# Kernel tuning notes

Hardware: AMD Instinct MI355X
Metric: run time of the kernel (lower is better)

## Reference

```python
import jax, jax.numpy as jnp
import numpy as np
from jax import lax

B, L, D, E, K, H = 8, 1024, 256, 8, 2, 1024  # batch, seq(in_channel), in_dim, experts, top_k, out_channel/hidden
LMAX = L // 2  # largest expert input dim (factor i+2 = 2)
LENS = [L // (i + 2) for i in range(E)]


def setup_inputs() -> dict:
    key = jax.random.key(0)
    ks = jax.random.split(key, 12)
    x = jax.random.normal(ks[0], (B, L, D), dtype=jnp.float32)
    conv_ws = jax.random.normal(ks[1], (3, D, D, 3), dtype=jnp.float32) / np.sqrt(3 * D)
    conv_bs = jax.random.normal(ks[2], (3, D), dtype=jnp.float32) * 0.01
    fl_w = jax.random.normal(ks[3], (E, L), dtype=jnp.float32) / np.sqrt(L)
    fl_b = jax.random.normal(ks[4], (E,), dtype=jnp.float32) * 0.01
    # expert first-layer weights, zero-padded on input axis to LMAX (expert i uses L//(i+2) inputs)
    w1 = jax.random.normal(ks[5], (E, H, LMAX), dtype=jnp.float32) / np.sqrt(LMAX)
    col_mask = (np.arange(LMAX)[None, :] < np.array(LENS)[:, None]).astype(np.float32)  # [E, LMAX]
    w1 = w1 * jnp.asarray(col_mask)[:, None, :]
    b1 = jax.random.normal(ks[6], (E, H), dtype=jnp.float32) * 0.01
    w2 = jax.random.normal(ks[7], (E, H, H), dtype=jnp.float32) / np.sqrt(H)
    b2 = jax.random.normal(ks[8], (E, H), dtype=jnp.float32) * 0.01
    w3 = jax.random.normal(ks[9], (E, H, H), dtype=jnp.float32) / np.sqrt(H)
    b3 = jax.random.normal(ks[10], (E, H), dtype=jnp.float32) * 0.01
    return {"x": x, "conv_ws": conv_ws, "conv_bs": conv_bs, "fl_w": fl_w, "fl_b": fl_b,
            "w1": w1, "b1": b1, "w2": w2, "b2": b2, "w3": w3, "b3": b3}


def _gelu(v):
    return jax.nn.gelu(v, approximate=False)  # torch nn.GELU default is exact erf


def _forward(x, conv_ws, conv_bs, fl_w, fl_b, w1, b1, w2, b2, w3, b3):
    xt = jnp.transpose(x, (0, 2, 1))  # [B, D, L]
    # --- Router: 3 dilated causal-padded ('same') convs + GELU ---
    h = xt
    for i in range(3):
        d = 2 ** i
        h = lax.conv_general_dilated(h, conv_ws[i], window_strides=(1,), padding=[(d, d)],
                                     rhs_dilation=(d,), dimension_numbers=("NCH", "OIH", "NCH"))
        h = _gelu(h + conv_bs[i][None, :, None])
    logits = jax.nn.sigmoid(jnp.einsum("bdl,el->bde", h, fl_w) + fl_b)  # [B, D, E]
    prob = jax.nn.softmax(logits, axis=-1)
    top_val, top_idx = lax.top_k(prob, K)  # [B, D, K]
    top_val = top_val / jnp.sum(top_val, axis=-1, keepdims=True)
    # combine gate per expert: gates[b,d,e] = sum_k top_val * 1[top_idx==e]
    gates = jnp.sum(top_val[..., None] * jax.nn.one_hot(top_idx, E, dtype=top_val.dtype), axis=2)  # [B, D, E]
    # --- Per-expert downsample (avg_pool1d, kernel=stride=i+2), zero-padded to LMAX ---
    xs = []
    for i in range(E):
        f = i + 2
        Li = LENS[i]
        xd = xt[:, :, :Li * f].reshape(B, D, Li, f).mean(-1)  # [B, D, Li]
        xs.append(jnp.pad(xd, ((0, 0), (0, 0), (0, LMAX - Li))))
    xe = jnp.stack(xs)  # [E, B, D, LMAX]; pad cols align with zeroed w1 cols
    # --- Expert MLPs (dense compute, masked by gates; zero gate == token not routed) ---
    h1 = _gelu(jnp.einsum("ebdl,ehl->ebdh", xe, w1) + b1[:, None, None, :])
    h2 = _gelu(jnp.einsum("ebdh,egh->ebdg", h1, w2) + b2[:, None, None, :])
    h3 = jnp.einsum("ebdg,eog->ebdo", h2, w3) + b3[:, None, None, :]  # [E, B, D, H]
    out = jnp.einsum("ebdo,bde->bdo", h3, gates)  # scatter-add combine, [B, D, H]
    return jnp.transpose(out, (0, 2, 1))  # [B, L(out_channel), D]


def reference(x, conv_ws, conv_bs, fl_w, fl_b, w1, b1, w2, b2, w3, b3):
    return _forward(x, conv_ws, conv_bs, fl_w, fl_b, w1, b1, w2, b2, w3, b3)
```

## Files before the change

kernel.cpp:

```cpp
#include <hip/hip_runtime.h>
#include <math.h>

#define Bb 8
#define Ll 1024
#define Dd 256
#define Ee 8
#define Hh 1024
#define LMAXc 512
#define NTOK (Bb*Dd)
#define LPAD 1032
#define MAXTILES 72

typedef short bf16x8 __attribute__((ext_vector_type(8)));
typedef float f32x4 __attribute__((ext_vector_type(4)));
typedef unsigned short u16x8 __attribute__((ext_vector_type(8)));

__device__ __forceinline__ float gelu_f(float x) {
    return 0.5f * x * (1.0f + erff(x * 0.70710678118654752440f));
}
__device__ __forceinline__ unsigned short f2b(float x) {
    unsigned int u = __float_as_uint(x);
    return (unsigned short)((u + 0x7fffu + ((u >> 16) & 1u)) >> 16);
}
__device__ __forceinline__ float b2f(unsigned short h) {
    return __uint_as_float(((unsigned int)h) << 16);
}
__device__ __forceinline__ void gl_lds16(const void* g, void* l) {
    __builtin_amdgcn_global_load_lds((const __attribute__((address_space(1))) unsigned int*)g,
                                     (__attribute__((address_space(3))) unsigned int*)l, 16, 0, 0);
}
__device__ __forceinline__ void split_one4(const float* __restrict__ src,
                                           unsigned short* __restrict__ hi,
                                           unsigned short* __restrict__ lo, int idx) {
    float4 v = ((const float4*)src)[idx];
    ushort2 h01, h23, l01, l23;
    unsigned short h;
    h = f2b(v.x); h01.x = h; l01.x = f2b(v.x - b2f(h));
    h = f2b(v.y); h01.y = h; l01.y = f2b(v.y - b2f(h));
    h = f2b(v.z); h23.x = h; l23.x = f2b(v.z - b2f(h));
    h = f2b(v.w); h23.y = h; l23.y = f2b(v.w - b2f(h));
    ((ushort2*)hi)[idx * 2] = h01; ((ushort2*)hi)[idx * 2 + 1] = h23;
    ((ushort2*)lo)[idx * 2] = l01; ((ushort2*)lo)[idx * 2 + 1] = l23;
}
__device__ __forceinline__ void cvt_one4(const float* __restrict__ src,
                                         unsigned short* __restrict__ dst, int idx) {
    float4 v = ((const float4*)src)[idx];
    ushort2 h01, h23;
    h01.x = f2b(v.x); h01.y = f2b(v.y);
    h23.x = f2b(v.z); h23.y = f2b(v.w);
    ((ushort2*)dst)[idx * 2] = h01; ((ushort2*)dst)[idx * 2 + 1] = h23;
}

__global__ __launch_bounds__(256) void prep_all(
    const float* __restrict__ x, const float* __restrict__ cw,
    const float* __restrict__ w1, const float* __restrict__ w2,
    const float* __restrict__ w3,
    unsigned short* __restrict__ xhi, unsigned short* __restrict__ xlo,
    unsigned short* __restrict__ chi, unsigned short* __restrict__ clo,
    unsigned short* __restrict__ wchi, unsigned short* __restrict__ wclo,
    unsigned short* __restrict__ w1hi, unsigned short* __restrict__ w1lo,
    unsigned short* __restrict__ w2b, unsigned short* __restrict__ w3b)
{
    int blk = blockIdx.x;
    int t = threadIdx.x;
    if (blk < 2048) {
        int idx = blk * 256 + t;
        int d4 = idx & 63;
        int l  = (idx >> 6) & 1023;
        int b  = idx >> 16;
        float4 v = ((const float4*)x)[idx];
        size_t o = ((size_t)(b * LPAD + 4 + l) * Dd + d4 * 4) >> 1;
        ushort2 h01, h23, l01, l23;
        unsigned short h;
        h = f2b(v.x); h01.x = h; l01.x = f2b(v.x - b2f(h));
        h = f2b(v.y); h01.y = h; l01.y = f2b(v.y - b2f(h));
        h = f2b(v.z); h23.x = h; l23.x = f2b(v.z - b2f(h));
        h = f2b(v.w); h23.y = h; l23.y = f2b(v.w - b2f(h));
        ((ushort2*)xhi)[o] = h01; ((ushort2*)xhi)[o + 1] = h23;
        ((ushort2*)xlo)[o] = l01; ((ushort2*)xlo)[o + 1] = l23;
    } else if (blk < 4352) {
        int idx = (blk - 2048) * 256 + t;
        int i = idx & (Dd - 1);
        int o = (idx >> 8) & (Dd - 1);
        int lk = idx >> 16;
        int layer = lk / 3;
        int k = lk % 3;
        float v = cw[(((size_t)layer * Dd + o) * Dd + i) * 3 + k];
        unsigned short h = f2b(v);
        wchi[idx] = h;
        wclo[idx] = f2b(v - b2f(h));
    } else if (blk < 8448) {
        split_one4(w1, w1hi, w1lo, (blk - 4352) * 256 + t);
    } else if (blk < 16640) {
        cvt_one4(w2, w2b, (blk - 8448) * 256 + t);
    } else if (blk < 24832) {
        cvt_one4(w3, w3b, (blk - 16640) * 256 + t);
    } else {
        int u = (blk - 24832) * 256 + t;
        int f = u >> 11;
        int rem = u & 2047;
        int b = rem >> 8;
        int r2 = rem & 255;
        int row = r2 >> 5;
        int col = (r2 & 31) * 8;
        int padrow = (row < 4) ? row : (1024 + row);
        unsigned short* buf = (f == 0) ? xhi : (f == 1) ? xlo : (f == 2) ? chi : clo;
        u16x8 z = {0, 0, 0, 0, 0, 0, 0, 0};
        *(u16x8*)(buf + (size_t)(b * LPAD + padrow) * Dd + col) = z;
    }
}

template<int MODE>
__global__ __launch_bounds__(256, 2) void conv_mfma(
    const unsigned short* __restrict__ inhi, const unsigned short* __restrict__ inlo,
    const unsigned short* __restrict__ whiL, const unsigned short* __restrict__ wloL,
    const float* __restrict__ bias,
    unsigned short* __restrict__ outhi, unsigned short* __restrict__ outlo,
    float* __restrict__ outf, int dil)
{
    __shared__ char smem[32768];
    char* sAhi = smem;
    char* sAlo = smem + 8192;
    char* sBhi = smem + 16384;
    char* sBlo = smem + 24576;

    const int t = threadIdx.x;
    const int lane = t & 63, w = t >> 6;
    const int r16 = lane & 15, quad = lane >> 4;
    const int wr = w >> 1, wc = w & 1;
    const int row0 = blockIdx.x * 64;
    const int col0 = blockIdx.y * 64;
    const int b = row0 >> 10, l0 = row0 & 1023;

    int aoff[2], boff[2];
    #pragma unroll
    for (int i = 0; i < 2; ++i) {
        int ra = wr * 32 + i * 16 + r16;
        aoff[i] = ra * 64 + ((quad ^ ((ra >> 1) & 3)) << 4);
        int rb = wc * 32 + i * 16 + r16;
        boff[i] = rb * 64 + ((quad ^ ((rb >> 1) & 3)) << 4);
    }
    const int rs = t >> 2, ce = ((t & 3) ^ ((rs >> 1) & 3)) << 3;
    const unsigned short* gAhi = inhi + (size_t)(b * LPAD + 4 + l0 + rs) * Dd + ce;
    const unsigned short* gAlo = inlo + (size_t)(b * LPAD + 4 + l0 + rs) * Dd + ce;

    f32x4 acc[2][2];
    const f32x4 zero4 = {0.f, 0.f, 0.f, 0.f};
    #pragma unroll
    for (int i = 0; i < 2; ++i)
        #pragma unroll
        for (int j = 0; j < 2; ++j) acc[i][j] = zero4;

    for (int tap = 0; tap < 3; ++tap) {
        const int sh = (tap - 1) * dil;
        const unsigned short* pAhi = gAhi + sh * Dd;
        const unsigned short* pAlo = gAlo + sh * Dd;
        const unsigned short* gBhi = whiL + ((size_t)tap * Dd + col0 + rs) * Dd + ce;
        const unsigned short* gBlo = wloL + ((size_t)tap * Dd + col0 + rs) * Dd + ce;
        for (int kb = 0; kb < Dd; kb += 64) {
            gl_lds16(pAhi + kb,      sAhi + (w << 10));
            gl_lds16(pAhi + kb + 32, sAhi + 4096 + (w << 10));
            gl_lds16(pAlo + kb,      sAlo + (w << 10));
            gl_lds16(pAlo + kb + 32, sAlo + 4096 + (w << 10));
            gl_lds16(gBhi + kb,      sBhi + (w << 10));
            gl_lds16(gBhi + kb + 32, sBhi + 4096 + (w << 10));
            gl_lds16(gBlo + kb,      sBlo + (w << 10));
            gl_lds16(gBlo + kb + 32, sBlo + 4096 + (w << 10));
            __syncthreads();
            #pragma unroll
            for (int h = 0; h < 2; ++h) {
                const int ho = h * 4096;
                bf16x8 ah[2], al[2], bh[2], bl[2];
                #pragma unroll
                for (int i = 0; i < 2; ++i) {
                    ah[i] = *(const bf16x8*)(sAhi + ho + aoff[i]);
                    al[i] = *(const bf16x8*)(sAlo + ho + aoff[i]);
                    bh[i] = *(const bf16x8*)(sBhi + ho + boff[i]);
                    bl[i] = *(const bf16x8*)(sBlo + ho + boff[i]);
                }
                #pragma unroll
                for (int mi = 0; mi < 2; ++mi)
                    #pragma unroll
                    for (int ni = 0; ni < 2; ++ni) {
                        acc[mi][ni] = __builtin_amdgcn_mfma_f32_16x16x32_bf16(ah[mi], bh[ni], acc[mi][ni], 0, 0, 0);
                        acc[mi][ni] = __builtin_amdgcn_mfma_f32_16x16x32_bf16(ah[mi], bl[ni], acc[mi][ni], 0, 0, 0);
                        acc[mi][ni] = __builtin_amdgcn_mfma_f32_16x16x32_bf16(al[mi], bh[ni], acc[mi][ni], 0, 0, 0);
                    }
            }
            __syncthreads();
        }
    }

    int cc[2]; float bv[2];
    #pragma unroll
    for (int ni = 0; ni < 2; ++ni) {
        cc[ni] = col0 + wc * 32 + ni * 16 + r16;
        bv[ni] = bias[cc[ni]];
    }
    #pragma unroll
    for (int mi = 0; mi < 2; ++mi) {
        int lb = l0 + wr * 32 + mi * 16 + quad * 4;
        #pragma unroll
        for (int reg = 0; reg < 4; ++reg) {
            int l = lb + reg;
            #pragma unroll
            for (int ni = 0; ni < 2; ++ni) {
                float v = gelu_f(acc[mi][ni][reg] + bv[ni]);
                if (MODE == 0) {
                    size_t o = (size_t)(b * LPAD + 4 + l) * Dd + cc[ni];
                    unsigned short h = f2b(v);
                    outhi[o] = h;
                    outlo[o] = f2b(v - b2f(h));
                } else {
                    outf[(size_t)(b * Ll + l) * Dd + cc[ni]] = v;
                }
            }
        }
    }
}

template<int MODE, int GATHER, int TWOPASS>
__global__ __launch_bounds__(256, 4) void gemm_sp(
    const unsigned short* __restrict__ AG,
    const unsigned short* __restrict__ BhiG, const unsigned short* __restrict__ BloG,
    const float* __restrict__ biasG, const float* __restrict__ gates,
    const int* __restrict__ cntG, const int* __restrict__ listG,
    const int* __restrict__ tileTab, const int* __restrict__ ntiles,
    unsigned short* __restrict__ Cout, float* __restrict__ outf,
    int M, int N, int K)
{
    if (blockIdx.y >= ntiles[0]) return;
    const int desc = tileTab[blockIdx.y];
    const int e = desc >> 16;
    const int row0 = (desc & 0xffff) * 64;
    const int cn = cntG[e];

    __shared__ char smem[TWOPASS ? 40960 : 24576];
    char* sA   = smem;
    char* sBhi = smem + 8192;
    char* sBlo = smem + 24576;

    const unsigned short* Bhi = BhiG + (size_t)e * N * K;
    const unsigned short* Blo = TWOPASS ? (BloG + (size_t)e * N * K) : nullptr;
    const float* bias = biasG + (size_t)e * N;

    const int t = threadIdx.x;
    const int lane = t & 63, w = t >> 6;
    const int r16 = lane & 15, quad = lane >> 4;
    const int wr = w >> 1, wc = w & 1;
    const int col0 = blockIdx.x * 128;

    int aoff[2], boff[4];
    #pragma unroll
    for (int i = 0; i < 2; ++i) {
        int ra = wr * 32 + i * 16 + r16;
        aoff[i] = ra * 64 + ((quad ^ ((ra >> 1) & 3)) << 4);
    }
    #pragma unroll
    for (int j = 0; j < 4; ++j) {
        int rb = wc * 64 + j * 16 + r16;
        boff[j] = rb * 64 + ((quad ^ ((rb >> 1) & 3)) << 4);
    }
    const int r0s = t >> 2, c0s = ((t & 3) ^ ((r0s >> 1) & 3)) << 3;
    const int r1s = r0s + 64, c1s = ((t & 3) ^ ((r1s >> 1) & 3)) << 3;
    int ri = row0 + r0s; if (ri > cn - 1) ri = cn - 1;
    const int ar = GATHER ? listG[e * NTOK + ri] : ri;
    const unsigned short* gA  = AG + ((size_t)e * M + ar) * K + c0s;
    const unsigned short* gBhi0 = Bhi + (size_t)(col0 + r0s) * K + c0s;
    const unsigned short* gBhi1 = Bhi + (size_t)(col0 + r1s) * K + c1s;
    const unsigned short* gBlo0 = TWOPASS ? (Blo + (size_t)(col0 + r0s) * K + c0s) : nullptr;
    const unsigned short* gBlo1 = TWOPASS ? (Blo + (size_t)(col0 + r1s) * K + c1s) : nullptr;
    const int wofs = w << 10;

    f32x4 acc[2][4];
    const f32x4 zero4 = {0.f, 0.f, 0.f, 0.f};
    #pragma unroll
    for (int i = 0; i < 2; ++i)
        #pragma unroll
        for (int j = 0; j < 4; ++j) acc[i][j] = zero4;

    for (int k0 = 0; k0 < K; k0 += 64) {
        gl_lds16(gA + k0,          sA + wofs);
        gl_lds16(gA + k0 + 32,     sA + 4096 + wofs);
        gl_lds16(gBhi0 + k0,       sBhi + wofs);
        gl_lds16(gBhi1 + k0,       sBhi + 4096 + wofs);
        gl_lds16(gBhi0 + k0 + 32,  sBhi + 8192 + wofs);
        gl_lds16(gBhi1 + k0 + 32,  sBhi + 12288 + wofs);
        if (TWOPASS) {
            gl_lds16(gBlo0 + k0,       sBlo + wofs);
            gl_lds16(gBlo1 + k0,       sBlo + 4096 + wofs);
            gl_lds16(gBlo0 + k0 + 32,  sBlo + 8192 + wofs);
            gl_lds16(gBlo1 + k0 + 32,  sBlo + 12288 + wofs);
        }
        __syncthreads();
        #pragma unroll
        for (int h = 0; h < 2; ++h) {
            const int ao = h * 4096, bo = h * 8192;
            bf16x8 ah[2], bh[4];
            #pragma unroll
            for (int i = 0; i < 2; ++i) ah[i] = *(const bf16x8*)(sA + ao + aoff[i]);
            #pragma unroll
            for (int j = 0; j < 4; ++j) bh[j] = *(const bf16x8*)(sBhi + bo + boff[j]);
            #pragma unroll
            for (int mi = 0; mi < 2; ++mi)
                #pragma unroll
                for (int ni = 0; ni < 4; ++ni)
                    acc[mi][ni] = __builtin_amdgcn_mfma_f32_16x16x32_bf16(ah[mi], bh[ni], acc[mi][ni], 0, 0, 0);
            if (TWOPASS) {
                bf16x8 bl[4];
                #pragma unroll
                for (int j = 0; j < 4; ++j) bl[j] = *(const bf16x8*)(sBlo + bo + boff[j]);
                #pragma unroll
                for (int mi = 0; mi < 2; ++mi)
                    #pragma unroll
                    for (int ni = 0; ni < 4; ++ni)
                        acc[mi][ni] = __builtin_amdgcn_mfma_f32_16x16x32_bf16(ah[mi], bl[ni], acc[mi][ni], 0, 0, 0);
            }
        }
        __syncthreads();
    }

    int cc[4]; float bv[4];
    #pragma unroll
    for (int ni = 0; ni < 4; ++ni) {
        cc[ni] = col0 + wc * 64 + ni * 16 + r16;
        bv[ni] = bias[cc[ni]];
    }
    if (MODE == 0) {
        unsigned short* CE = Cout + (size_t)e * M * N;
        #pragma unroll
        for (int mi = 0; mi < 2; ++mi) {
            int rb = row0 + wr * 32 + mi * 16 + quad * 4;
            #pragma unroll
            for (int reg = 0; reg < 4; ++reg) {
                size_t roff = (size_t)(rb + reg) * N;
                #pragma unroll
                for (int ni = 0; ni < 4; ++ni)
                    CE[roff + cc[ni]] = f2b(gelu_f(acc[mi][ni][reg] + bv[ni]));
            }
        }
    } else {
        #pragma unroll
        for (int mi = 0; mi < 2; ++mi) {
            int rb = row0 + wr * 32 + mi * 16 + quad * 4;
            #pragma unroll
            for (int reg = 0; reg < 4; ++reg) {
                int i = rb + reg;
                if (i < cn) {
                    int tok = listG[e * NTOK + i];
                    float g = gates[(size_t)tok * Ee + e];
                    size_t roff = (size_t)tok * N;
                    #pragma unroll
                    for (int ni = 0; ni < 4; ++ni)
                        atomicAdd(&outf[roff + cc[ni]], g * (acc[mi][ni][reg] + bv[ni]));
                }
            }
        }
    }
}


__global__ __launch_bounds__(256) void logits_accum(const float* __restrict__ h,
                                                    const float* __restrict__ fl_w,
                                                    float* __restrict__ logits) {
    int b = blockIdx.x;
    int chunk = blockIdx.y;
    __shared__ float wsm[Ee][128];
    for (int i = threadIdx.x; i < Ee * 128; i += 256) {
        int e = i >> 7, l = i & 127;
        wsm[e][l] = fl_w[e * Ll + chunk * 128 + l];
    }
    __syncthreads();
    int d = threadIdx.x;
    float acc[Ee] = {};
    for (int l = 0; l < 128; ++l) {
        float v = h[((size_t)b * Ll + chunk * 128 + l) * Dd + d];
        #pragma unroll
        for (int e = 0; e < Ee; ++e) acc[e] += v * wsm[e][l];
    }
    int tok = b * Dd + d;
    #pragma unroll
    for (int e = 0; e < Ee; ++e) atomicAdd(&logits[tok * Ee + e], acc[e]);
}

__global__ __launch_bounds__(1024) void gates_final(const float* __restrict__ logits,
                                                    const float* __restrict__ fl_b,
                                                    float* __restrict__ gates,
                                                    int* __restrict__ cnt,
                                                    int* __restrict__ list,
                                                    int* __restrict__ tileTab,
                                                    int* __restrict__ ntiles) {
    for (int tok = threadIdx.x; tok < NTOK; tok += 1024) {
        float s[Ee];
        #pragma unroll
        for (int e = 0; e < Ee; ++e) {
            float z = logits[tok * Ee + e] + fl_b[e];
            s[e] = 1.0f / (1.0f + expf(-z));
        }
        float mx = s[0];
        #pragma unroll
        for (int e = 1; e < Ee; ++e) mx = fmaxf(mx, s[e]);
        float p[Ee];
        #pragma unroll
        for (int e = 0; e < Ee; ++e) p[e] = expf(s[e] - mx);
        int i1 = 0;
        #pragma unroll
        for (int e = 1; e < Ee; ++e) if (p[e] > p[i1]) i1 = e;
        int i2 = (i1 == 0) ? 1 : 0;
        #pragma unroll
        for (int e = 0; e < Ee; ++e) {
            if (e == i1 || e == i2) continue;
            if (p[e] > p[i2]) i2 = e;
        }
        float inv = 1.0f / (p[i1] + p[i2]);
        #pragma unroll
        for (int e = 0; e < Ee; ++e) gates[tok * Ee + e] = 0.0f;
        gates[tok * Ee + i1] = p[i1] * inv;
        gates[tok * Ee + i2] = p[i2] * inv;
        int p1 = atomicAdd(&cnt[i1], 1);
        list[i1 * NTOK + p1] = tok;
        int p2 = atomicAdd(&cnt[i2], 1);
        list[i2 * NTOK + p2] = tok;
    }
    __syncthreads();
    if (threadIdx.x == 0) {
        int nt = 0;
        for (int e = 0; e < Ee; ++e) {
            int c = atomicAdd(&cnt[e], 0);
            for (int m = 0; m * 64 < c; ++m) tileTab[nt++] = (e << 16) | m;
        }
        ntiles[0] = nt;
    }
}

__global__ __launch_bounds__(256) void downsample_v3(const float* __restrict__ x,
                                                     unsigned short* __restrict__ xe) {
    int e = blockIdx.z;
    int f = e + 2;
    int Li = Ll / f;
    int j0 = blockIdx.x * 8;
    if (j0 >= Li) return;
    int b = blockIdx.y;
    int d = threadIdx.x;
    float invf = 1.0f / (float)f;
    int lim = Li - 1;
    float v[8] = {};
    for (int r = 0; r < f; ++r) {
        #pragma unroll
        for (int jj = 0; jj < 8; ++jj) {
            int j = j0 + jj; if (j > lim) j = lim;
            v[jj] += x[((size_t)(b * Ll + j * f + r)) * Dd + d];
        }
    }
    size_t obase = ((size_t)(e * NTOK + b * 256 + d)) * LMAXc + j0;
    if (j0 + 8 <= Li) {
        u16x8 hv;
        #pragma unroll
        for (int q = 0; q < 8; ++q) hv[q] = (short)f2b(v[q] * invf);
        *(u16x8*)(xe + obase) = hv;
    } else {
        for (int jj = 0; jj < Li - j0; ++jj)
            xe[obase + jj] = f2b(v[jj] * invf);
    }
}

__global__ __launch_bounds__(256) void transpose_out(const float* __restrict__ outacc,
                                                     float* __restrict__ out) {
    __shared__ float tile[32][33];
    int b = blockIdx.z;
    int d0 = blockIdx.x * 32;
    int o0 = blockIdx.y * 32;
    int tx = threadIdx.x & 31, ty = threadIdx.x >> 5;
    for (int i = 0; i < 32; i += 8)
        tile[ty + i][tx] = outacc[((size_t)b * Dd + d0 + ty + i) * Hh + o0 + tx];
    __syncthreads();
    for (int i = 0; i < 32; i += 8)
        out[((size_t)b * Hh + o0 + ty + i) * Dd + d0 + tx] = tile[tx][ty + i];
}

extern "C" void kernel_launch(void* const* d_in, const int* in_sizes, int n_in,
                              void* d_out, int out_size, void* d_ws, size_t ws_size,
                              hipStream_t stream) {
    const float* x       = (const float*)d_in[0];
    const float* conv_w  = (const float*)d_in[1];
    const float* conv_b  = (const float*)d_in[2];
    const float* fl_w    = (const float*)d_in[3];
    const float* fl_b    = (const float*)d_in[4];
    const float* w1      = (const float*)d_in[5];
    const float* b1      = (const float*)d_in[6];
    const float* w2      = (const float*)d_in[7];
    const float* b2      = (const float*)d_in[8];
    const float* w3      = (const float*)d_in[9];
    const float* b3      = (const float*)d_in[10];
    float* out = (float*)d_out;

    char* ws = (char*)d_ws;
    unsigned short* xphi = (unsigned short*)(ws);
    unsigned short* xplo = (unsigned short*)(ws + 4227072);
    unsigned short* cphi = (unsigned short*)(ws + 8454144);
    unsigned short* cplo = (unsigned short*)(ws + 12681216);
    unsigned short* wchi = (unsigned short*)(ws + 16908288);
    unsigned short* wclo = (unsigned short*)(ws + 18087936);
    float* hL            = (float*)(ws + 19267584);
    unsigned short* h1   = (unsigned short*)(ws);
    unsigned short* h2   = (unsigned short*)(ws + 33554432);
    unsigned short* xe   = (unsigned short*)(ws + 67108864);
    unsigned short* w1hi = (unsigned short*)(ws + 83886080);
    unsigned short* w1lo = (unsigned short*)(ws + 92274688);
    unsigned short* w2b  = (unsigned short*)(ws + 100663296);
    unsigned short* w3b  = (unsigned short*)(ws + 117440512);
    float* logits  = (float*)(ws + 134217728);
    int*   cnt     = (int*)(ws + 134283264);
    int*   ntiles  = (int*)(ws + 134283296);
    int*   tileTab = (int*)(ws + 134283328);
    float* gates   = (float*)(ws + 134284288);
    int*   list    = (int*)(ws + 134349824);
    float* outacc  = (float*)(ws);

    hipMemsetAsync(logits, 0, 65536 + 64, stream);

    prep_all<<<24864, 256, 0, stream>>>(x, conv_w, w1, w2, w3,
                                        xphi, xplo, cphi, cplo, wchi, wclo,
                                        w1hi, w1lo, w2b, w3b);

    const int WL = 3 * Dd * Dd;
    conv_mfma<0><<<dim3(Bb * Ll / 64, Dd / 64), 256, 0, stream>>>(
        xphi, xplo, wchi + 0 * WL, wclo + 0 * WL, conv_b + 0 * Dd, cphi, cplo, nullptr, 1);
    conv_mfma<0><<<dim3(Bb * Ll / 64, Dd / 64), 256, 0, stream>>>(
        cphi, cplo, wchi + 1 * WL, wclo + 1 * WL, conv_b + 1 * Dd, xphi, xplo, nullptr, 2);
    conv_mfma<1><<<dim3(Bb * Ll / 64, Dd / 64), 256, 0, stream>>>(
        xphi, xplo, wchi + 2 * WL, wclo + 2 * WL, conv_b + 2 * Dd, nullptr, nullptr, hL, 4);

    logits_accum<<<dim3(Bb, 8), 256, 0, stream>>>(hL, fl_w, logits);
    gates_final<<<1, 1024, 0, stream>>>(logits, fl_b, gates, cnt, list, tileTab, ntiles);

    downsample_v3<<<dim3(64, Bb, Ee), 256, 0, stream>>>(x, xe);

    gemm_sp<0, 1, 1><<<dim3(Hh / 128, MAXTILES), 256, 0, stream>>>(
        xe, w1hi, w1lo, b1, nullptr, cnt, list, tileTab, ntiles, h1, nullptr, NTOK, Hh, LMAXc);

    gemm_sp<0, 0, 0><<<dim3(Hh / 128, MAXTILES), 256, 0, stream>>>(
        h1, w2b, nullptr, b2, nullptr, cnt, list, tileTab, ntiles, h2, nullptr, NTOK, Hh, Hh);

    hipMemsetAsync(outacc, 0, (size_t)NTOK * Hh * sizeof(float), stream);

    gemm_sp<1, 0, 0><<<dim3(Hh / 128, MAXTILES), 256, 0, stream>>>(
        h2, w3b, nullptr, b3, gates, cnt, list, tileTab, ntiles, nullptr, outacc, NTOK, Hh, Hh);

    transpose_out<<<dim3(Dd / 32, Hh / 32, Bb), 256, 0, stream>>>(outacc, out);
}
```

Baseline: 329.1 us.

## Halve expert GEMM column tile and aggregate routing atomics per wavefront

The expert GEMM kernels now use 64x64 output tiles instead of 64x128, doubling the grid width to 16 column blocks so more workgroups are available for the sparse tile count. Shared memory per block shrinks accordingly. The routing kernel replaces per-token global atomics with wavefront ballot aggregation into shared-memory counters, writing the counts out once at the end. The smaller tile gives less B-operand reuse per A load and doubles A-tile reloads.

```diff
diff --git a/kernel.cpp b/kernel.cpp
--- a/kernel.cpp
+++ b/kernel.cpp
@@ -235,10 +235,10 @@
     const int row0 = (desc & 0xffff) * 64;
     const int cn = cntG[e];
 
-    __shared__ char smem[TWOPASS ? 40960 : 24576];
+    __shared__ char smem[TWOPASS ? 24576 : 16384];
     char* sA   = smem;
     char* sBhi = smem + 8192;
-    char* sBlo = smem + 24576;
+    char* sBlo = smem + 16384;
 
     const unsigned short* Bhi = BhiG + (size_t)e * N * K;
     const unsigned short* Blo = TWOPASS ? (BloG + (size_t)e * N * K) : nullptr;
@@ -248,82 +248,73 @@
     const int lane = t & 63, w = t >> 6;
     const int r16 = lane & 15, quad = lane >> 4;
     const int wr = w >> 1, wc = w & 1;
-    const int col0 = blockIdx.x * 128;
-
-    int aoff[2], boff[4];
+    const int col0 = blockIdx.x * 64;
+
+    int aoff[2], boff[2];
     #pragma unroll
     for (int i = 0; i < 2; ++i) {
         int ra = wr * 32 + i * 16 + r16;
         aoff[i] = ra * 64 + ((quad ^ ((ra >> 1) & 3)) << 4);
-    }
-    #pragma unroll
-    for (int j = 0; j < 4; ++j) {
-        int rb = wc * 64 + j * 16 + r16;
-        boff[j] = rb * 64 + ((quad ^ ((rb >> 1) & 3)) << 4);
+        int rb = wc * 32 + i * 16 + r16;
+        boff[i] = rb * 64 + ((quad ^ ((rb >> 1) & 3)) << 4);
     }
     const int r0s = t >> 2, c0s = ((t & 3) ^ ((r0s >> 1) & 3)) << 3;
-    const int r1s = r0s + 64, c1s = ((t & 3) ^ ((r1s >> 1) & 3)) << 3;
     int ri = row0 + r0s; if (ri > cn - 1) ri = cn - 1;
     const int ar = GATHER ? listG[e * NTOK + ri] : ri;
     const unsigned short* gA  = AG + ((size_t)e * M + ar) * K + c0s;
-    const unsigned short* gBhi0 = Bhi + (size_t)(col0 + r0s) * K + c0s;
-    const unsigned short* gBhi1 = Bhi + (size_t)(col0 + r1s) * K + c1s;
-    const unsigned short* gBlo0 = TWOPASS ? (Blo + (size_t)(col0 + r0s) * K + c0s) : nullptr;
-    const unsigned short* gBlo1 = TWOPASS ? (Blo + (size_t)(col0 + r1s) * K + c1s) : nullptr;
+    const unsigned short* gB  = Bhi + (size_t)(col0 + r0s) * K + c0s;
+    const unsigned short* gBl = TWOPASS ? (Blo + (size_t)(col0 + r0s) * K + c0s) : nullptr;
     const int wofs = w << 10;
 
-    f32x4 acc[2][4];
+    f32x4 acc[2][2];
     const f32x4 zero4 = {0.f, 0.f, 0.f, 0.f};
     #pragma unroll
     for (int i = 0; i < 2; ++i)
         #pragma unroll
-        for (int j = 0; j < 4; ++j) acc[i][j] = zero4;
+        for (int j = 0; j < 2; ++j) acc[i][j] = zero4;
 
     for (int k0 = 0; k0 < K; k0 += 64) {
-        gl_lds16(gA + k0,          sA + wofs);
-        gl_lds16(gA + k0 + 32,     sA + 4096 + wofs);
-        gl_lds16(gBhi0 + k0,       sBhi + wofs);
-        gl_lds16(gBhi1 + k0,       sBhi + 4096 + wofs);
-        gl_lds16(gBhi0 + k0 + 32,  sBhi + 8192 + wofs);
-        gl_lds16(gBhi1 + k0 + 32,  sBhi + 12288 + wofs);
+        gl_lds16(gA + k0,        sA + wofs);
+        gl_lds16(gA + k0 + 32,   sA + 4096 + wofs);
+        gl_lds16(gB + k0,        sBhi + wofs);
+        gl_lds16(gB + k0 + 32,   sBhi + 4096 + wofs);
         if (TWOPASS) {
-            gl_lds16(gBlo0 + k0,       sBlo + wofs);
-            gl_lds16(gBlo1 + k0,       sBlo + 4096 + wofs);
-            gl_lds16(gBlo0 + k0 + 32,  sBlo + 8192 + wofs);
-            gl_lds16(gBlo1 + k0 + 32,  sBlo + 12288 + wofs);
+            gl_lds16(gBl + k0,      sBlo + wofs);
+            gl_lds16(gBl + k0 + 32, sBlo + 4096 + wofs);
         }
         __syncthreads();
         #pragma unroll
         for (int h = 0; h < 2; ++h) {
-            const int ao = h * 4096, bo = h * 8192;
-            bf16x8 ah[2], bh[4];
+            const int ho = h * 4096;
+            bf16x8 ah[2], bh[2];
             #pragma unroll
-            for (int i = 0; i < 2; ++i) ah[i] = *(const bf16x8*)(sA + ao + aoff[i]);
-            #pragma unroll
-            for (int j = 0; j < 4; ++j) bh[j] = *(const bf16x8*)(sBhi + bo + boff[j]);
+            for (int i = 0; i < 2; ++i) {
+                ah[i] = *(const bf16x8*)(sA + ho + aoff[i]);
+                bh[i] = *(const bf16x8*)(sBhi + ho + boff[i]);
+            }
             #pragma unroll
             for (int mi = 0; mi < 2; ++mi)
                 #pragma unroll
-                for (int ni = 0; ni < 4; ++ni)
+                for (int ni = 0; ni < 2; ++ni)
                     acc[mi][ni] = __builtin_amdgcn_mfma_f32_16x16x32_bf16(ah[mi], bh[ni], acc[mi][ni], 0, 0, 0);
             if (TWOPASS) {
-                bf16x8 bl[4];
+                bf16x8 bl[2];
                 #pragma unroll
-                for (int j = 0; j < 4; ++j) bl[j] = *(const bf16x8*)(sBlo + bo + boff[j]);
+                for (int i = 0; i < 2; ++i) bl[i] = *(const bf16x8*)(sBlo + ho + boff[i]);
                 #pragma unroll
                 for (int mi = 0; mi < 2; ++mi)
                     #pragma unroll
-                    for (int ni = 0; ni < 4; ++ni)
+                    for (int ni = 0; ni < 2; ++ni)
                         acc[mi][ni] = __builtin_amdgcn_mfma_f32_16x16x32_bf16(ah[mi], bl[ni], acc[mi][ni], 0, 0, 0);
             }
         }
         __syncthreads();
     }
 
-    int cc[4]; float bv[4];
-    #pragma unroll
-    for (int ni = 0; ni < 4; ++ni) {
-        cc[ni] = col0 + wc * 64 + ni * 16 + r16;
+    int cc[2]; float bv[2];
+    #pragma unroll
+    for (int ni = 0; ni < 2; ++ni) {
+        cc[ni] = col0 + wc * 32 + ni * 16 + r16;
         bv[ni] = bias[cc[ni]];
     }
     if (MODE == 0) {
@@ -335,7 +326,7 @@
             for (int reg = 0; reg < 4; ++reg) {
                 size_t roff = (size_t)(rb + reg) * N;
                 #pragma unroll
-                for (int ni = 0; ni < 4; ++ni)
+                for (int ni = 0; ni < 2; ++ni)
                     CE[roff + cc[ni]] = f2b(gelu_f(acc[mi][ni][reg] + bv[ni]));
             }
         }
@@ -351,7 +342,7 @@
                     float g = gates[(size_t)tok * Ee + e];
                     size_t roff = (size_t)tok * N;
                     #pragma unroll
-                    for (int ni = 0; ni < 4; ++ni)
+                    for (int ni = 0; ni < 2; ++ni)
                         atomicAdd(&outf[roff + cc[ni]], g * (acc[mi][ni][reg] + bv[ni]));
                 }
             }
@@ -390,6 +381,12 @@
                                                     int* __restrict__ list,
                                                     int* __restrict__ tileTab,
                                                     int* __restrict__ ntiles) {
+    __shared__ int scnt[Ee];
+    if (threadIdx.x < Ee) scnt[threadIdx.x] = 0;
+    __syncthreads();
+    const int lane = threadIdx.x & 63;
+    const unsigned long long ltmask = (1ull << lane) - 1ull;
+
     for (int tok = threadIdx.x; tok < NTOK; tok += 1024) {
         float s[Ee];
         #pragma unroll
@@ -417,16 +414,31 @@
         for (int e = 0; e < Ee; ++e) gates[tok * Ee + e] = 0.0f;
         gates[tok * Ee + i1] = p[i1] * inv;
         gates[tok * Ee + i2] = p[i2] * inv;
-        int p1 = atomicAdd(&cnt[i1], 1);
-        list[i1 * NTOK + p1] = tok;
-        int p2 = atomicAdd(&cnt[i2], 1);
-        list[i2 * NTOK + p2] = tok;
+
+        #pragma unroll
+        for (int slot = 0; slot < 2; ++slot) {
+            int ie = slot ? i2 : i1;
+            for (int e = 0; e < Ee; ++e) {
+                unsigned long long m = __ballot(ie == e);
+                if (m) {
+                    int leader = __ffsll((long long)m) - 1;
+                    int base = 0;
+                    if (lane == leader) base = atomicAdd(&scnt[e], (int)__popcll(m));
+                    base = __shfl(base, leader);
+                    if (ie == e) {
+                        int pos = base + (int)__popcll(m & ltmask);
+                        list[e * NTOK + pos] = tok;
+                    }
+                }
+            }
+        }
     }
     __syncthreads();
+    if (threadIdx.x < Ee) cnt[threadIdx.x] = scnt[threadIdx.x];
     if (threadIdx.x == 0) {
         int nt = 0;
         for (int e = 0; e < Ee; ++e) {
-            int c = atomicAdd(&cnt[e], 0);
+            int c = scnt[e];
             for (int m = 0; m * 64 < c; ++m) tileTab[nt++] = (e << 16) | m;
         }
         ntiles[0] = nt;
@@ -536,15 +548,15 @@
 
     downsample_v3<<<dim3(64, Bb, Ee), 256, 0, stream>>>(x, xe);
 
-    gemm_sp<0, 1, 1><<<dim3(Hh / 128, MAXTILES), 256, 0, stream>>>(
+    gemm_sp<0, 1, 1><<<dim3(16, MAXTILES), 256, 0, stream>>>(
         xe, w1hi, w1lo, b1, nullptr, cnt, list, tileTab, ntiles, h1, nullptr, NTOK, Hh, LMAXc);
 
-    gemm_sp<0, 0, 0><<<dim3(Hh / 128, MAXTILES), 256, 0, stream>>>(
+    gemm_sp<0, 0, 0><<<dim3(16, MAXTILES), 256, 0, stream>>>(
         h1, w2b, nullptr, b2, nullptr, cnt, list, tileTab, ntiles, h2, nullptr, NTOK, Hh, Hh);
 
     hipMemsetAsync(outacc, 0, (size_t)NTOK * Hh * sizeof(float), stream);
 
-    gemm_sp<1, 0, 0><<<dim3(Hh / 128, MAXTILES), 256, 0, stream>>>(
+    gemm_sp<1, 0, 0><<<dim3(16, MAXTILES), 256, 0, stream>>>(
         h2, w3b, nullptr, b3, gates, cnt, list, tileTab, ntiles, nullptr, outacc, NTOK, Hh, Hh);
 
     transpose_out<<<dim3(Dd / 32, Hh / 32, Bb), 256, 0, stream>>>(outacc, out);
```

Result: faster. 320.2 us (-2.7%).
